# Optimization experiments

Hardware: AMD Instinct MI355X
Metric: run time of the kernel (lower is better)

The kernel has to match this reference:

```python
import jax, jax.numpy as jnp
import numpy as np
from jax import lax

DIM = 96
B, H, W = 4, 256, 256


def setup_inputs() -> dict:
    key = jax.random.key(0)
    ks = jax.random.split(key, 20)
    f = lambda k, s, scale=0.05: (jax.random.normal(k, s, dtype=jnp.float32) * scale)
    d = DIM
    return {
        "x": jax.random.normal(ks[0], (B, d, H, W), dtype=jnp.float32),
        "prompt": jax.random.normal(ks[1], (B, d), dtype=jnp.float32),
        "scale_weights": jax.random.uniform(ks[2], (B, 3), dtype=jnp.float32),
        "ln_w": jnp.ones((d,), jnp.float32),
        "ln_b": jnp.zeros((d,), jnp.float32),
        "e0_pw_w": f(ks[3], (d, d)),       # expert0 pointwise 1x1: [out, in]
        "e0_pw_b": f(ks[4], (d,)),
        "e0_dw_w": f(ks[5], (d, 1, 3, 3)),  # depthwise 3x3
        "e0_dw_b": f(ks[6], (d,)),
        "e1_dw_w": f(ks[7], (d, 1, 3, 3)),  # depthwise 3x3, dilation 2
        "e1_dw_b": f(ks[8], (d,)),
        "e2_dw_w": f(ks[9], (d, 1, 5, 5)),  # depthwise 5x5, dilation 3
        "e2_dw_b": f(ks[10], (d,)),
        "proj_w": f(ks[11], (d, d)),
        "proj_b": f(ks[12], (d,)),
        "ffn1_w": f(ks[13], (2 * d, d)),
        "ffn1_b": f(ks[14], (2 * d,)),
        "ffn2_w": f(ks[15], (d, 2 * d)),
        "ffn2_b": f(ks[16], (d,)),
    }


def _conv1x1(x, w, b):
    # x: [B,C,H,W], w: [O,C]
    return jnp.einsum('bchw,oc->bohw', x, w) + b[None, :, None, None]


def _dwconv(x, w, b, dilation, pad):
    # depthwise conv, w: [C,1,k,k]
    c = x.shape[1]
    y = lax.conv_general_dilated(
        x, w, window_strides=(1, 1),
        padding=[(pad, pad), (pad, pad)],
        rhs_dilation=(dilation, dilation),
        feature_group_count=c,
        dimension_numbers=('NCHW', 'OIHW', 'NCHW'))
    return y + b[None, :, None, None]


def _layernorm_c(x, w, b, eps=1e-6):
    # LayerNorm over channel dim of NCHW (torch permutes to NHWC, norms last dim)
    mu = jnp.mean(x, axis=1, keepdims=True)
    var = jnp.mean((x - mu) ** 2, axis=1, keepdims=True)
    xn = (x - mu) * lax.rsqrt(var + eps)
    return xn * w[None, :, None, None] + b[None, :, None, None]


def reference(x, prompt, scale_weights, ln_w, ln_b,
              e0_pw_w, e0_pw_b, e0_dw_w, e0_dw_b,
              e1_dw_w, e1_dw_b, e2_dw_w, e2_dw_b,
              proj_w, proj_b, ffn1_w, ffn1_b, ffn2_w, ffn2_b):
    shortcut = x
    xn = _layernorm_c(x, ln_w, ln_b)

    # Three receptive-field experts (all run densely, soft-weighted)
    e0 = _dwconv(_conv1x1(xn, e0_pw_w, e0_pw_b), e0_dw_w, e0_dw_b, dilation=1, pad=1)
    e1 = _dwconv(xn, e1_dw_w, e1_dw_b, dilation=2, pad=2)
    e2 = _dwconv(xn, e2_dw_w, e2_dw_b, dilation=3, pad=6)

    w = scale_weights  # [B,3]
    x_adaptive = (w[:, 0, None, None, None] * e0
                  + w[:, 1, None, None, None] * e1
                  + w[:, 2, None, None, None] * e2)
    x_adaptive = x_adaptive * (1.0 + prompt[:, :, None, None])

    x1 = shortcut + _conv1x1(x_adaptive, proj_w, proj_b)
    h = jax.nn.gelu(_conv1x1(x1, ffn1_w, ffn1_b), approximate=False)
    out = x1 + _conv1x1(h, ffn2_w, ffn2_b)
    return out
```

## Files before the change

kernel.cpp:

```cpp
#include <hip/hip_runtime.h>
#include <hip/hip_bf16.h>

typedef __hip_bfloat16 bf16;
typedef __attribute__((ext_vector_type(8))) __bf16 bf16x8;
typedef __attribute__((ext_vector_type(4))) float  f32x4;

#define HW   65536
#define WID  256
#define CC   96
#define NB   4
static const size_t S_ELEMS = (size_t)NB * CC * HW;

__device__ __forceinline__ float lo2f(unsigned u) { unsigned x = u << 16;        return __builtin_bit_cast(float, x); }
__device__ __forceinline__ float hi2f(unsigned u) { unsigned x = u & 0xffff0000u; return __builtin_bit_cast(float, x); }
__device__ __forceinline__ unsigned short f2bu(float f) {
    return __builtin_bit_cast(unsigned short, __float2bfloat16(f));
}

__device__ __forceinline__ void store8b(bf16* p, const float v[8]) {
    alignas(16) bf16 o[8];
#pragma unroll
    for (int i = 0; i < 8; ++i) o[i] = __float2bfloat16(v[i]);
    *reinterpret_cast<uint4*>(p) = *reinterpret_cast<const uint4*>(o);
}

__device__ __forceinline__ float gelu_erf(float v) {
    float z  = fabsf(v) * 0.70710678118654752f;
    float t  = __builtin_amdgcn_rcpf(1.f + 0.3275911f * z);
    float poly = t * (0.254829592f + t * (-0.284496736f + t * (1.421413741f
               + t * (-1.453152027f + t * 1.061405429f))));
    float erfz = 1.f - poly * __expf(-z * z);
    float erfv = copysignf(erfz, v);
    return 0.5f * v * (1.f + erfv);
}

__global__ __launch_bounds__(256) void ln_kernel(
    const float* __restrict__ x, const float* __restrict__ lw,
    const float* __restrict__ lb, bf16* __restrict__ y)
{
    int t  = blockIdx.x * 256 + threadIdx.x;
    int b  = t >> 15;
    int hw = (t & 32767) * 2;
    size_t base = (size_t)b * CC * HW + hw;

    float s0 = 0.f, s1 = 0.f, q0 = 0.f, q1 = 0.f;
    for (int c = 0; c < CC; ++c) {
        float2 v = *reinterpret_cast<const float2*>(&x[base + (size_t)c * HW]);
        s0 += v.x; s1 += v.y; q0 += v.x * v.x; q1 += v.y * v.y;
    }
    float mu0 = s0 * (1.f / 96.f), mu1 = s1 * (1.f / 96.f);
    float rs0 = rsqrtf(q0 * (1.f / 96.f) - mu0 * mu0 + 1e-6f);
    float rs1 = rsqrtf(q1 * (1.f / 96.f) - mu1 * mu1 + 1e-6f);

    for (int c = 0; c < CC; ++c) {
        float2 v = *reinterpret_cast<const float2*>(&x[base + (size_t)c * HW]);
        float g = lw[c], be = lb[c];
        bf16 o[2];
        o[0] = __float2bfloat16((v.x - mu0) * rs0 * g + be);
        o[1] = __float2bfloat16((v.y - mu1) * rs1 * g + be);
        *reinterpret_cast<uint*>(&y[base + (size_t)c * HW]) = *reinterpret_cast<uint*>(o);
    }
}

__device__ __forceinline__ int swzo(int row, int col, int width) {
    return (row * width + col) ^ ((((row & 7) ^ ((row >> 3) & 7)) << 3));
}

template <typename TI, typename TOT, int CIN, int COUT, bool GELU, bool HASRES>
__global__ __launch_bounds__(256) void conv1x1_mfma(
    const TI* __restrict__ in, const float* __restrict__ wgt,
    const float* __restrict__ bias, const float* __restrict__ resid,
    TOT* __restrict__ out)
{
    constexpr int MT     = COUT / 16;
    constexpr int KSPLIT = CIN / 96;
    constexpr int CS     = 96;
    static_assert(CIN == KSPLIT * CS, "CIN must be 96 or 192");

    __shared__ unsigned short s_w[COUT * CIN];
    __shared__ unsigned short s_x[128 * CS];
    __shared__ float          s_b[COUT];

    const int tid  = threadIdx.x;
    const int lane = tid & 63;
    const int wave = tid >> 6;
    const int q    = lane >> 4;
    const int n    = lane & 15;

    const int pos0 = blockIdx.x * 128;
    const int b    = pos0 >> 16;
    const int hw0  = pos0 & 65535;

    constexpr int C4 = CIN / 4;
    for (int k = tid; k < COUT * C4; k += 256) {
        int o = k / C4, c4 = (k - o * C4) * 4;
        float4 w4 = *reinterpret_cast<const float4*>(&wgt[o * CIN + c4]);
        ushort4 pk = make_ushort4(f2bu(w4.x), f2bu(w4.y), f2bu(w4.z), f2bu(w4.w));
        *reinterpret_cast<ushort4*>(&s_w[swzo(o, c4, CIN)]) = pk;
    }
    for (int k = tid; k < COUT; k += 256) s_b[k] = bias[k];

    const TI* inb = in + (size_t)b * CIN * HW;

    f32x4 acc[MT][2];
#pragma unroll
    for (int mt = 0; mt < MT; ++mt) {
        acc[mt][0] = {0.f, 0.f, 0.f, 0.f};
        acc[mt][1] = {0.f, 0.f, 0.f, 0.f};
    }

    const int pl0 = wave * 32 + n;
    const int pl1 = pl0 + 16;

#pragma unroll
    for (int ks = 0; ks < KSPLIT; ++ks) {
        if (ks) __syncthreads();

        for (int idx = tid; idx < CS * 16; idx += 256) {
            const int c    = idx >> 4;
            const int pblk = idx & 15;
            const int row0 = pblk * 8;
            const TI* gp = inb + (size_t)(ks * CS + c) * HW + hw0 + row0;
            alignas(16) unsigned short u[8];
            if constexpr (__is_same(TI, float)) {
                float4 a  = *reinterpret_cast<const float4*>(gp);
                float4 b2 = *reinterpret_cast<const float4*>(gp + 4);
                u[0] = f2bu(a.x);  u[1] = f2bu(a.y);  u[2] = f2bu(a.z);  u[3] = f2bu(a.w);
                u[4] = f2bu(b2.x); u[5] = f2bu(b2.y); u[6] = f2bu(b2.z); u[7] = f2bu(b2.w);
            } else {
                *reinterpret_cast<uint4*>(u) = *reinterpret_cast<const uint4*>(gp);
            }
#pragma unroll
            for (int i = 0; i < 8; ++i)
                s_x[swzo(row0 + i, c, CS)] = u[i];
        }
        __syncthreads();

#pragma unroll
        for (int kt = 0; kt < CS / 32; ++kt) {
            const int col = kt * 32 + q * 8;
            union { unsigned short u[8]; bf16x8 v; } bf0, bf1;
            *reinterpret_cast<uint4*>(bf0.u) =
                *reinterpret_cast<const uint4*>(&s_x[swzo(pl0, col, CS)]);
            *reinterpret_cast<uint4*>(bf1.u) =
                *reinterpret_cast<const uint4*>(&s_x[swzo(pl1, col, CS)]);
#pragma unroll
            for (int mt = 0; mt < MT; ++mt) {
                union { unsigned short u[8]; bf16x8 v; } fa;
                *reinterpret_cast<uint4*>(fa.u) =
                    *reinterpret_cast<const uint4*>(&s_w[swzo(mt * 16 + n, ks * CS + col, CIN)]);
                acc[mt][0] = __builtin_amdgcn_mfma_f32_16x16x32_bf16(fa.v, bf0.v, acc[mt][0], 0, 0, 0);
                acc[mt][1] = __builtin_amdgcn_mfma_f32_16x16x32_bf16(fa.v, bf1.v, acc[mt][1], 0, 0, 0);
            }
        }
    }

    const int p0 = hw0 + pl0;
    const int p1 = hw0 + pl1;
    const size_t obase = (size_t)b * COUT * HW;
#pragma unroll
    for (int mt = 0; mt < MT; ++mt) {
#pragma unroll
        for (int nt = 0; nt < 2; ++nt) {
            const int p = (nt == 0) ? p0 : p1;
#pragma unroll
            for (int r = 0; r < 4; ++r) {
                const int o = mt * 16 + q * 4 + r;
                float v = acc[mt][nt][r] + s_b[o];
                if constexpr (GELU) v = gelu_erf(v);
                const size_t idx = obase + (size_t)o * HW + p;
                if constexpr (HASRES) v += resid[idx];
                if constexpr (__is_same(TOT, float)) out[idx] = v;
                else                                 out[idx] = __float2bfloat16(v);
            }
        }
    }
}

#define LW 272
#define XROWS 20
#define TROWS 10

__device__ __forceinline__ void load_win24_lds(const unsigned short* s, float win[24])
{
    uint4 c0 = *reinterpret_cast<const uint4*>(s);
    uint4 c1 = *reinterpret_cast<const uint4*>(s + 8);
    uint4 c2 = *reinterpret_cast<const uint4*>(s + 16);
    win[0]=lo2f(c0.x); win[1]=hi2f(c0.x); win[2]=lo2f(c0.y); win[3]=hi2f(c0.y);
    win[4]=lo2f(c0.z); win[5]=hi2f(c0.z); win[6]=lo2f(c0.w); win[7]=hi2f(c0.w);
    win[8]=lo2f(c1.x); win[9]=hi2f(c1.x); win[10]=lo2f(c1.y); win[11]=hi2f(c1.y);
    win[12]=lo2f(c1.z); win[13]=hi2f(c1.z); win[14]=lo2f(c1.w); win[15]=hi2f(c1.w);
    win[16]=lo2f(c2.x); win[17]=hi2f(c2.x); win[18]=lo2f(c2.y); win[19]=hi2f(c2.y);
    win[20]=lo2f(c2.z); win[21]=hi2f(c2.z); win[22]=lo2f(c2.w); win[23]=hi2f(c2.w);
}
__device__ __forceinline__ void apply3(const float wk[3], int dil,
                                       const float win[24], float acc[8])
{
#pragma unroll
    for (int kw = 0; kw < 3; ++kw) {
        float wv = wk[kw];
        int d = (kw - 1) * dil;
#pragma unroll
        for (int o = 0; o < 8; ++o) acc[o] += wv * win[o + 8 + d];
    }
}
__device__ __forceinline__ void apply5(const float wk[5],
                                       const float win[24], float acc[8])
{
#pragma unroll
    for (int kw = 0; kw < 5; ++kw) {
        float wv = wk[kw];
        int d = (kw - 2) * 3;
#pragma unroll
        for (int o = 0; o < 8; ++o) acc[o] += wv * win[o + 8 + d];
    }
}

__global__ __launch_bounds__(256) void experts_kernel(
    const bf16* __restrict__ xn, const bf16* __restrict__ t0,
    const float* __restrict__ w0, const float* __restrict__ b0,
    const float* __restrict__ w1, const float* __restrict__ b1,
    const float* __restrict__ w2, const float* __restrict__ b2,
    const float* __restrict__ sw, const float* __restrict__ prompt,
    bf16* __restrict__ xa)
{
    __shared__ unsigned short sx[XROWS * LW];
    __shared__ unsigned short st[TROWS * LW];

    const int tid = threadIdx.x;
    const int bid = blockIdx.x;
    const int h0  = (bid & 31) * 8;
    const int bc  = bid >> 5;
    const int b   = bc / 96;
    const int c   = bc - b * 96;
    const size_t pbase = (size_t)bc * HW;

    const bf16* xp = xn + pbase;
    const bf16* tp = t0 + pbase;

    const uint4 z4 = make_uint4(0u, 0u, 0u, 0u);
    for (int idx = tid; idx < XROWS * 34; idx += 256) {
        int row = idx / 34, ch = idx - row * 34;
        int gh  = h0 - 6 + row;
        uint4 v = z4;
        if (ch >= 1 && ch <= 32 && (unsigned)gh < 256u)
            v = *reinterpret_cast<const uint4*>(xp + gh * WID + (ch - 1) * 8);
        *reinterpret_cast<uint4*>(&sx[row * LW + ch * 8]) = v;
    }
    for (int idx = tid; idx < TROWS * 34; idx += 256) {
        int row = idx / 34, ch = idx - row * 34;
        int gh  = h0 - 1 + row;
        uint4 v = z4;
        if (ch >= 1 && ch <= 32 && (unsigned)gh < 256u)
            v = *reinterpret_cast<const uint4*>(tp + gh * WID + (ch - 1) * 8);
        *reinterpret_cast<uint4*>(&st[row * LW + ch * 8]) = v;
    }

    float wk0[9], wk1[9], wk2[25];
#pragma unroll
    for (int i = 0; i < 9; ++i)  wk0[i] = w0[c * 9 + i];
#pragma unroll
    for (int i = 0; i < 9; ++i)  wk1[i] = w1[c * 9 + i];
#pragma unroll
    for (int i = 0; i < 25; ++i) wk2[i] = w2[c * 25 + i];

    __syncthreads();

    const int wg  = tid & 31;
    const int r   = tid >> 5;
    const int h   = h0 + r;
    const int w0p = wg * 8;

    float acc0[8], acc1[8], acc2[8];
    {
        float bb0 = b0[c], bb1 = b1[c], bb2 = b2[c];
#pragma unroll
        for (int o = 0; o < 8; ++o) { acc0[o] = bb0; acc1[o] = bb1; acc2[o] = bb2; }
    }

    float win[24];
    load_win24_lds(&sx[(r + 0)  * LW + w0p], win); apply5(&wk2[0],  win, acc2);
    load_win24_lds(&sx[(r + 3)  * LW + w0p], win); apply5(&wk2[5],  win, acc2);
    load_win24_lds(&sx[(r + 4)  * LW + w0p], win); apply3(&wk1[0], 2, win, acc1);
    load_win24_lds(&sx[(r + 6)  * LW + w0p], win);
    apply3(&wk1[3], 2, win, acc1); apply5(&wk2[10], win, acc2);
    load_win24_lds(&sx[(r + 8)  * LW + w0p], win); apply3(&wk1[6], 2, win, acc1);
    load_win24_lds(&sx[(r + 9)  * LW + w0p], win); apply5(&wk2[15], win, acc2);
    load_win24_lds(&sx[(r + 12) * LW + w0p], win); apply5(&wk2[20], win, acc2);
    load_win24_lds(&st[(r + 0) * LW + w0p], win); apply3(&wk0[0], 1, win, acc0);
    load_win24_lds(&st[(r + 1) * LW + w0p], win); apply3(&wk0[3], 1, win, acc0);
    load_win24_lds(&st[(r + 2) * LW + w0p], win); apply3(&wk0[6], 1, win, acc0);

    float s0 = sw[b * 3 + 0], s1 = sw[b * 3 + 1], s2 = sw[b * 3 + 2];
    float pr = 1.f + prompt[b * 96 + c];
    float ov[8];
#pragma unroll
    for (int o = 0; o < 8; ++o)
        ov[o] = (s0 * acc0[o] + s1 * acc1[o] + s2 * acc2[o]) * pr;
    store8b(&xa[pbase + h * WID + w0p], ov);
}

extern "C" void kernel_launch(void* const* d_in, const int* in_sizes, int n_in,
                              void* d_out, int out_size, void* d_ws, size_t ws_size,
                              hipStream_t stream)
{
    const float* x       = (const float*)d_in[0];
    const float* prompt  = (const float*)d_in[1];
    const float* sw      = (const float*)d_in[2];
    const float* ln_w    = (const float*)d_in[3];
    const float* ln_b    = (const float*)d_in[4];
    const float* e0_pw_w = (const float*)d_in[5];
    const float* e0_pw_b = (const float*)d_in[6];
    const float* e0_dw_w = (const float*)d_in[7];
    const float* e0_dw_b = (const float*)d_in[8];
    const float* e1_dw_w = (const float*)d_in[9];
    const float* e1_dw_b = (const float*)d_in[10];
    const float* e2_dw_w = (const float*)d_in[11];
    const float* e2_dw_b = (const float*)d_in[12];
    const float* proj_w  = (const float*)d_in[13];
    const float* proj_b  = (const float*)d_in[14];
    const float* ffn1_w  = (const float*)d_in[15];
    const float* ffn1_b  = (const float*)d_in[16];
    const float* ffn2_w  = (const float*)d_in[17];
    const float* ffn2_b  = (const float*)d_in[18];

    float* out = (float*)d_out;
    bf16*  ws  = (bf16*)d_ws;
    bf16*  A   = ws;
    bf16*  Bt  = ws + S_ELEMS;
    bf16*  Cx  = ws + 2 * S_ELEMS;
    bf16*  E   = ws;

    ln_kernel<<<512, 256, 0, stream>>>(x, ln_w, ln_b, A);
    conv1x1_mfma<bf16, bf16, 96, 96, false, false>
        <<<2048, 256, 0, stream>>>(A, e0_pw_w, e0_pw_b, nullptr, Bt);
    experts_kernel<<<12288, 256, 0, stream>>>(A, Bt, e0_dw_w, e0_dw_b, e1_dw_w, e1_dw_b,
                                              e2_dw_w, e2_dw_b, sw, prompt, Cx);
    conv1x1_mfma<bf16, float, 96, 96, false, true>
        <<<2048, 256, 0, stream>>>(Cx, proj_w, proj_b, x, out);
    conv1x1_mfma<float, bf16, 96, 192, true, false>
        <<<2048, 256, 0, stream>>>(out, ffn1_w, ffn1_b, nullptr, E);
    conv1x1_mfma<bf16, float, 192, 96, false, true>
        <<<2048, 256, 0, stream>>>(E, ffn2_w, ffn2_b, out, out);
}
```

Baseline: 517.0 us.

## Transpose expert depthwise-conv LDS tiles to column-major, one thread per column

The experts kernel now stores its input halo tiles transposed in LDS (column-major with a small pitch), and each thread computes 8 vertical outputs for one column instead of 8 horizontal outputs for one row. Every thread gets a contiguous column strip, so LDS reads become narrower 32-bit loads reused across kernel rows. In exchange it adds scalar 16-bit transposed LDS stores, an explicit zero-fill pass with an extra barrier, and scattered 2-byte global stores of the outputs instead of 16-byte vector stores.

```diff
diff --git a/kernel.cpp b/kernel.cpp
--- a/kernel.cpp
+++ b/kernel.cpp
@@ -15,13 +15,6 @@
 __device__ __forceinline__ float hi2f(unsigned u) { unsigned x = u & 0xffff0000u; return __builtin_bit_cast(float, x); }
 __device__ __forceinline__ unsigned short f2bu(float f) {
     return __builtin_bit_cast(unsigned short, __float2bfloat16(f));
-}
-
-__device__ __forceinline__ void store8b(bf16* p, const float v[8]) {
-    alignas(16) bf16 o[8];
-#pragma unroll
-    for (int i = 0; i < 8; ++i) o[i] = __float2bfloat16(v[i]);
-    *reinterpret_cast<uint4*>(p) = *reinterpret_cast<const uint4*>(o);
 }
 
 __device__ __forceinline__ float gelu_erf(float v) {
@@ -177,44 +170,12 @@
     }
 }
 
-#define LW 272
-#define XROWS 20
-#define TROWS 10
-
-__device__ __forceinline__ void load_win24_lds(const unsigned short* s, float win[24])
-{
-    uint4 c0 = *reinterpret_cast<const uint4*>(s);
-    uint4 c1 = *reinterpret_cast<const uint4*>(s + 8);
-    uint4 c2 = *reinterpret_cast<const uint4*>(s + 16);
-    win[0]=lo2f(c0.x); win[1]=hi2f(c0.x); win[2]=lo2f(c0.y); win[3]=hi2f(c0.y);
-    win[4]=lo2f(c0.z); win[5]=hi2f(c0.z); win[6]=lo2f(c0.w); win[7]=hi2f(c0.w);
-    win[8]=lo2f(c1.x); win[9]=hi2f(c1.x); win[10]=lo2f(c1.y); win[11]=hi2f(c1.y);
-    win[12]=lo2f(c1.z); win[13]=hi2f(c1.z); win[14]=lo2f(c1.w); win[15]=hi2f(c1.w);
-    win[16]=lo2f(c2.x); win[17]=hi2f(c2.x); win[18]=lo2f(c2.y); win[19]=hi2f(c2.y);
-    win[20]=lo2f(c2.z); win[21]=hi2f(c2.z); win[22]=lo2f(c2.w); win[23]=hi2f(c2.w);
-}
-__device__ __forceinline__ void apply3(const float wk[3], int dil,
-                                       const float win[24], float acc[8])
-{
-#pragma unroll
-    for (int kw = 0; kw < 3; ++kw) {
-        float wv = wk[kw];
-        int d = (kw - 1) * dil;
-#pragma unroll
-        for (int o = 0; o < 8; ++o) acc[o] += wv * win[o + 8 + d];
-    }
-}
-__device__ __forceinline__ void apply5(const float wk[5],
-                                       const float win[24], float acc[8])
-{
-#pragma unroll
-    for (int kw = 0; kw < 5; ++kw) {
-        float wv = wk[kw];
-        int d = (kw - 2) * 3;
-#pragma unroll
-        for (int o = 0; o < 8; ++o) acc[o] += wv * win[o + 8 + d];
-    }
-}
+#define XR     20
+#define TRW    10
+#define XPITCH 22
+#define TPITCH 10
+#define XCOLS  268
+#define TCOLS  258
 
 __global__ __launch_bounds__(256) void experts_kernel(
     const bf16* __restrict__ xn, const bf16* __restrict__ t0,
@@ -224,8 +185,8 @@
     const float* __restrict__ sw, const float* __restrict__ prompt,
     bf16* __restrict__ xa)
 {
-    __shared__ unsigned short sx[XROWS * LW];
-    __shared__ unsigned short st[TROWS * LW];
+    __shared__ alignas(16) unsigned short sxT[XCOLS * XPITCH];
+    __shared__ alignas(16) unsigned short stT[TCOLS * TPITCH];
 
     const int tid = threadIdx.x;
     const int bid = blockIdx.x;
@@ -235,69 +196,124 @@
     const int c   = bc - b * 96;
     const size_t pbase = (size_t)bc * HW;
 
+    {
+        uint* zx = reinterpret_cast<uint*>(sxT);
+        for (int i = tid; i < XCOLS * XPITCH / 2; i += 256) zx[i] = 0u;
+        uint* zt = reinterpret_cast<uint*>(stT);
+        for (int i = tid; i < TCOLS * TPITCH / 2; i += 256) zt[i] = 0u;
+    }
+
+    float wk0[9], wk1[9], wk2[25];
+#pragma unroll
+    for (int i = 0; i < 9; ++i)  wk0[i] = w0[c * 9 + i];
+#pragma unroll
+    for (int i = 0; i < 9; ++i)  wk1[i] = w1[c * 9 + i];
+#pragma unroll
+    for (int i = 0; i < 25; ++i) wk2[i] = w2[c * 25 + i];
+    const float bb0 = b0[c], bb1 = b1[c], bb2 = b2[c];
+    const float s0 = sw[b * 3 + 0], s1 = sw[b * 3 + 1], s2 = sw[b * 3 + 2];
+    const float pr = 1.f + prompt[b * 96 + c];
+
+    __syncthreads();
+
     const bf16* xp = xn + pbase;
     const bf16* tp = t0 + pbase;
-
-    const uint4 z4 = make_uint4(0u, 0u, 0u, 0u);
-    for (int idx = tid; idx < XROWS * 34; idx += 256) {
-        int row = idx / 34, ch = idx - row * 34;
-        int gh  = h0 - 6 + row;
-        uint4 v = z4;
-        if (ch >= 1 && ch <= 32 && (unsigned)gh < 256u)
-            v = *reinterpret_cast<const uint4*>(xp + gh * WID + (ch - 1) * 8);
-        *reinterpret_cast<uint4*>(&sx[row * LW + ch * 8]) = v;
-    }
-    for (int idx = tid; idx < TROWS * 34; idx += 256) {
-        int row = idx / 34, ch = idx - row * 34;
-        int gh  = h0 - 1 + row;
-        uint4 v = z4;
-        if (ch >= 1 && ch <= 32 && (unsigned)gh < 256u)
-            v = *reinterpret_cast<const uint4*>(tp + gh * WID + (ch - 1) * 8);
-        *reinterpret_cast<uint4*>(&st[row * LW + ch * 8]) = v;
-    }
-
-    float wk0[9], wk1[9], wk2[25];
-#pragma unroll
-    for (int i = 0; i < 9; ++i)  wk0[i] = w0[c * 9 + i];
-#pragma unroll
-    for (int i = 0; i < 9; ++i)  wk1[i] = w1[c * 9 + i];
-#pragma unroll
-    for (int i = 0; i < 25; ++i) wk2[i] = w2[c * 25 + i];
-
+    for (int idx = tid; idx < XR * 32; idx += 256) {
+        const int row = idx >> 5, ch = idx & 31;
+        const int gh  = h0 - 6 + row;
+        if ((unsigned)gh < 256u) {
+            union { uint4 q; unsigned short u[8]; } v;
+            v.q = *reinterpret_cast<const uint4*>(xp + gh * WID + ch * 8);
+            const int base = (6 + ch * 8) * XPITCH + row;
+#pragma unroll
+            for (int i = 0; i < 8; ++i) sxT[base + i * XPITCH] = v.u[i];
+        }
+    }
+    for (int idx = tid; idx < TRW * 32; idx += 256) {
+        const int row = idx >> 5, ch = idx & 31;
+        const int gh  = h0 - 1 + row;
+        if ((unsigned)gh < 256u) {
+            union { uint4 q; unsigned short u[8]; } v;
+            v.q = *reinterpret_cast<const uint4*>(tp + gh * WID + ch * 8);
+            const int base = (1 + ch * 8) * TPITCH + row;
+#pragma unroll
+            for (int i = 0; i < 8; ++i) stT[base + i * TPITCH] = v.u[i];
+        }
+    }
     __syncthreads();
 
-    const int wg  = tid & 31;
-    const int r   = tid >> 5;
-    const int h   = h0 + r;
-    const int w0p = wg * 8;
-
+    const int w = tid;
     float acc0[8], acc1[8], acc2[8];
-    {
-        float bb0 = b0[c], bb1 = b1[c], bb2 = b2[c];
-#pragma unroll
-        for (int o = 0; o < 8; ++o) { acc0[o] = bb0; acc1[o] = bb1; acc2[o] = bb2; }
-    }
-
-    float win[24];
-    load_win24_lds(&sx[(r + 0)  * LW + w0p], win); apply5(&wk2[0],  win, acc2);
-    load_win24_lds(&sx[(r + 3)  * LW + w0p], win); apply5(&wk2[5],  win, acc2);
-    load_win24_lds(&sx[(r + 4)  * LW + w0p], win); apply3(&wk1[0], 2, win, acc1);
-    load_win24_lds(&sx[(r + 6)  * LW + w0p], win);
-    apply3(&wk1[3], 2, win, acc1); apply5(&wk2[10], win, acc2);
-    load_win24_lds(&sx[(r + 8)  * LW + w0p], win); apply3(&wk1[6], 2, win, acc1);
-    load_win24_lds(&sx[(r + 9)  * LW + w0p], win); apply5(&wk2[15], win, acc2);
-    load_win24_lds(&sx[(r + 12) * LW + w0p], win); apply5(&wk2[20], win, acc2);
-    load_win24_lds(&st[(r + 0) * LW + w0p], win); apply3(&wk0[0], 1, win, acc0);
-    load_win24_lds(&st[(r + 1) * LW + w0p], win); apply3(&wk0[3], 1, win, acc0);
-    load_win24_lds(&st[(r + 2) * LW + w0p], win); apply3(&wk0[6], 1, win, acc0);
-
-    float s0 = sw[b * 3 + 0], s1 = sw[b * 3 + 1], s2 = sw[b * 3 + 2];
-    float pr = 1.f + prompt[b * 96 + c];
-    float ov[8];
-#pragma unroll
-    for (int o = 0; o < 8; ++o)
-        ov[o] = (s0 * acc0[o] + s1 * acc1[o] + s2 * acc2[o]) * pr;
-    store8b(&xa[pbase + h * WID + w0p], ov);
+#pragma unroll
+    for (int r = 0; r < 8; ++r) { acc0[r] = bb0; acc1[r] = bb1; acc2[r] = bb2; }
+
+    const unsigned short* bx = &sxT[w * XPITCH];
+    const unsigned short* bt = &stT[w * TPITCH];
+
+#pragma unroll
+    for (int kw = 0; kw < 5; ++kw) {
+        float cv[20];
+#pragma unroll
+        for (int j = 0; j < 10; ++j) {
+            unsigned u = *reinterpret_cast<const unsigned*>(&bx[kw * 3 * XPITCH + 2 * j]);
+            cv[2 * j]     = lo2f(u);
+            cv[2 * j + 1] = hi2f(u);
+        }
+#pragma unroll
+        for (int kh = 0; kh < 5; ++kh) {
+            const float wv = wk2[kh * 5 + kw];
+#pragma unroll
+            for (int r = 0; r < 8; ++r) acc2[r] += wv * cv[r + 3 * kh];
+        }
+        if (kw == 2) {
+#pragma unroll
+            for (int kh = 0; kh < 3; ++kh) {
+                const float wv = wk1[kh * 3 + 1];
+#pragma unroll
+                for (int r = 0; r < 8; ++r) acc1[r] += wv * cv[r + 2 * kh + 4];
+            }
+        }
+    }
+#pragma unroll
+    for (int kwh = 0; kwh < 2; ++kwh) {
+        const int kw = kwh * 2;
+        float cv[12];
+#pragma unroll
+        for (int j = 0; j < 6; ++j) {
+            unsigned u = *reinterpret_cast<const unsigned*>(&bx[(4 + 2 * kw) * XPITCH + 4 + 2 * j]);
+            cv[2 * j]     = lo2f(u);
+            cv[2 * j + 1] = hi2f(u);
+        }
+#pragma unroll
+        for (int kh = 0; kh < 3; ++kh) {
+            const float wv = wk1[kh * 3 + kw];
+#pragma unroll
+            for (int r = 0; r < 8; ++r) acc1[r] += wv * cv[r + 2 * kh];
+        }
+    }
+#pragma unroll
+    for (int kw = 0; kw < 3; ++kw) {
+        float cv[10];
+#pragma unroll
+        for (int j = 0; j < 5; ++j) {
+            unsigned u = *reinterpret_cast<const unsigned*>(&bt[kw * TPITCH + 2 * j]);
+            cv[2 * j]     = lo2f(u);
+            cv[2 * j + 1] = hi2f(u);
+        }
+#pragma unroll
+        for (int kh = 0; kh < 3; ++kh) {
+            const float wv = wk0[kh * 3 + kw];
+#pragma unroll
+            for (int r = 0; r < 8; ++r) acc0[r] += wv * cv[r + kh];
+        }
+    }
+
+    bf16* op = xa + pbase + (size_t)h0 * WID + w;
+#pragma unroll
+    for (int r = 0; r < 8; ++r) {
+        float v = (s0 * acc0[r] + s1 * acc1[r] + s2 * acc2[r]) * pr;
+        op[r * WID] = __float2bfloat16(v);
+    }
 }
 
 extern "C" void kernel_launch(void* const* d_in, const int* in_sizes, int n_in,
```

After: 519.9 us. No clear change (+0.6%).
